# Optimization experiments

Hardware: AMD Instinct MI355X
Metric: run time of the kernel (lower is better)

The kernel has to match this reference:

```python
import jax, jax.numpy as jnp
import numpy as np

N, E, G = 100000, 1600000, 64
IN_DIM, EMB, HID, HEADS, OUT = 128, 128, 32, 4, 64
CAT = HID * HEADS  # 128
EPS = 1e-5
SLOPE = 0.2


def gat_conv(x, src, dst, W, a_src, a_dst, bias):
    # x: [N, F_in]; W: [HEADS*HID, F_in]; a_*: [1, HEADS, HID]; bias: [HEADS*HID]
    h = (x @ W.T).reshape(N, HEADS, HID)
    s_src = (h * a_src).sum(-1)  # [N, HEADS]
    s_dst = (h * a_dst).sum(-1)
    e = jax.nn.leaky_relu(s_src[src] + s_dst[dst], SLOPE)  # [Etot, HEADS]
    m = jax.ops.segment_max(e, dst, num_segments=N)
    p = jnp.exp(e - m[dst])
    denom = jax.ops.segment_sum(p, dst, num_segments=N)
    alpha = p / denom[dst]  # softmax over incoming edges per dst node
    out = jax.ops.segment_sum(h[src] * alpha[:, :, None], dst, num_segments=N)
    return out.reshape(N, CAT) + bias


def graph_norm(x, batch, w, b, mean_scale):
    cnt = jax.ops.segment_sum(jnp.ones((N,), x.dtype), batch, num_segments=G)[:, None]
    mean = jax.ops.segment_sum(x, batch, num_segments=G) / cnt  # [G, C]
    sub = x - mean_scale * mean[batch]
    var = jax.ops.segment_sum(sub * sub, batch, num_segments=G) / cnt
    inv = 1.0 / jnp.sqrt(var + EPS)
    return w * sub * inv[batch] + b


def setup_inputs() -> dict:
    key = jax.random.key(0)
    ks = jax.random.split(key, 20)
    g = lambda k, shape, s: jax.random.normal(k, shape, dtype=jnp.float32) * s
    inp = {
        'x': g(ks[0], (N, IN_DIM), 1.0),
        'edge_index': jax.random.randint(ks[1], (2, E), 0, N, dtype=jnp.int64 if jax.config.read('jax_enable_x64') else jnp.int32),
        'batch': jnp.sort(jax.random.randint(ks[2], (N,), 0, G)),
        'enc_w': g(ks[3], (EMB, IN_DIM), 0.08),
        'enc_b': jnp.zeros((EMB,), jnp.float32),
        'w1': g(ks[4], (HEADS * HID, EMB), 0.08),
        'att_src1': g(ks[5], (1, HEADS, HID), 0.15),
        'att_dst1': g(ks[6], (1, HEADS, HID), 0.15),
        'b1': jnp.zeros((CAT,), jnp.float32),
        'n1_w': jnp.ones((CAT,), jnp.float32),
        'n1_b': jnp.zeros((CAT,), jnp.float32),
        'n1_ms': jnp.ones((CAT,), jnp.float32),
        'w2': g(ks[7], (HEADS * HID, CAT), 0.08),
        'att_src2': g(ks[8], (1, HEADS, HID), 0.15),
        'att_dst2': g(ks[9], (1, HEADS, HID), 0.15),
        'b2': jnp.zeros((CAT,), jnp.float32),
        'n2_w': jnp.ones((CAT,), jnp.float32),
        'n2_b': jnp.zeros((CAT,), jnp.float32),
        'n2_ms': jnp.ones((CAT,), jnp.float32),
        'fc_w': g(ks[10], (OUT, CAT), 0.08),
        'fc_b': jnp.zeros((OUT,), jnp.float32),
    }
    return inp


def reference(x, edge_index, batch, enc_w, enc_b, w1, att_src1, att_dst1, b1,
              n1_w, n1_b, n1_ms, w2, att_src2, att_dst2, b2, n2_w, n2_b, n2_ms,
              fc_w, fc_b):
    # PyG GATConv adds self-loops by default
    loops = jnp.arange(N, dtype=edge_index.dtype)
    src = jnp.concatenate([edge_index[0], loops])
    dst = jnp.concatenate([edge_index[1], loops])

    h = x @ enc_w.T + enc_b
    h = jax.nn.elu(gat_conv(h, src, dst, w1, att_src1, att_dst1, b1))
    h = graph_norm(h, batch, n1_w, n1_b, n1_ms)  # dropout = identity (eval)
    h = jax.nn.elu(gat_conv(h, src, dst, w2, att_src2, att_dst2, b2))
    h = graph_norm(h, batch, n2_w, n2_b, n2_ms)
    pooled = jax.ops.segment_max(h, batch, num_segments=G)  # global_max_pool
    return pooled @ fc_w.T + fc_b  # out_dim != 1 -> no sigmoid
```

## Files before the change

### kernel.cpp

```cpp
#include <hip/hip_runtime.h>
#include <hip/hip_bf16.h>

#define SLOPE 0.2f
#define EPS_GN 1e-5f
#define APITCH 136
#define NBUCK 391

typedef __attribute__((ext_vector_type(8))) short bfrag;
typedef __attribute__((ext_vector_type(4))) float ffrag;

__device__ __forceinline__ float lrelu(float v) { return v > 0.f ? v : SLOPE * v; }
__device__ __forceinline__ unsigned int flipf(float x) {
    unsigned int u = __float_as_uint(x);
    return (u & 0x80000000u) ? ~u : (u | 0x80000000u);
}
__device__ __forceinline__ float unflipf(unsigned int u) {
    return __uint_as_float((u & 0x80000000u) ? (u & 0x7fffffffu) : ~u);
}
__device__ __forceinline__ short f2bs(float v) {
    __hip_bfloat16 h = __float2bfloat16(v);
    return *reinterpret_cast<short*>(&h);
}
__device__ __forceinline__ float bs2f(short s) {
    __hip_bfloat16 h = *reinterpret_cast<__hip_bfloat16*>(&s);
    return __bfloat162float(h);
}
__device__ __forceinline__ float blo(unsigned int u) { return __uint_as_float(u << 16); }
__device__ __forceinline__ float bhi(unsigned int u) { return __uint_as_float(u & 0xffff0000u); }

__global__ void zero_kernel(float* __restrict__ p, int n) {
    int i = blockIdx.x * 256 + threadIdx.x;
    if (i < n) p[i] = 0.f;
}

__global__ void prep_weights(const float* __restrict__ enc_w,
                             const float* __restrict__ enc_b,
                             const float* __restrict__ w1,
                             const float* __restrict__ w2,
                             unsigned short* __restrict__ WT1b,
                             unsigned short* __restrict__ WT2b,
                             float* __restrict__ bc1, float* __restrict__ bc2) {
    int c = blockIdx.x;
    int k = threadIdx.x;
    __shared__ float w1row[128];
    w1row[k] = w1[c * 128 + k];
    __syncthreads();
    float acc = 0.f;
    for (int j = 0; j < 128; ++j)
        acc = fmaf(w1row[j], enc_w[j * 128 + k], acc);
    WT1b[c * 128 + k] = (unsigned short)f2bs(acc);
    WT2b[c * 128 + k] = (unsigned short)f2bs(w2[c * 128 + k]);
    if (k == 0) {
        float b = 0.f;
        for (int j = 0; j < 128; ++j) b += w1row[j] * enc_b[j];
        bc1[c] = b;
        bc2[c] = 0.f;
    }
}


__global__ void __launch_bounds__(256) bucket_hist(const int* __restrict__ ei,
                                                   int* __restrict__ bhist, int E, int N) {
    __shared__ int h[NBUCK];
    for (int i = threadIdx.x; i < NBUCK; i += 256) h[i] = 0;
    __syncthreads();
    int base = blockIdx.x * 4096;
#pragma unroll
    for (int s = 0; s < 16; ++s) {
        int e = base + s * 256 + threadIdx.x;
        if (e < E + N) {
            int dst = (e < E) ? ei[E + e] : (e - E);
            atomicAdd(&h[dst >> 8], 1);
        }
    }
    __syncthreads();
    for (int i = threadIdx.x; i < NBUCK; i += 256)
        if (h[i]) atomicAdd(&bhist[i], h[i]);
}

__global__ void bucket_scan(const int* __restrict__ bhist,
                            int* __restrict__ bbase, int* __restrict__ bcur) {
    __shared__ int sh[512];
    int t = threadIdx.x;
    int v = (t < NBUCK) ? bhist[t] : 0;
    sh[t] = v;
    __syncthreads();
    for (int off = 1; off < 512; off <<= 1) {
        int add = (t >= off) ? sh[t - off] : 0;
        __syncthreads();
        sh[t] += add;
        __syncthreads();
    }
    if (t < NBUCK) {
        bbase[t] = sh[t] - v;
        bcur[t] = sh[t] - v;
    }
}

__global__ void __launch_bounds__(256) bucket_scatter(const int* __restrict__ ei,
                                                      int* __restrict__ bcur,
                                                      unsigned int* __restrict__ staging,
                                                      int E, int N) {
    __shared__ int h[NBUCK];
    __shared__ int lb[NBUCK];
    for (int i = threadIdx.x; i < NBUCK; i += 256) h[i] = 0;
    __syncthreads();
    int base = blockIdx.x * 4096;
    int srcv[16], dstv[16];
#pragma unroll
    for (int s = 0; s < 16; ++s) {
        int e = base + s * 256 + threadIdx.x;
        srcv[s] = -1;
        if (e < E + N) {
            srcv[s] = (e < E) ? ei[e] : (e - E);
            dstv[s] = (e < E) ? ei[E + e] : (e - E);
            atomicAdd(&h[dstv[s] >> 8], 1);
        }
    }
    __syncthreads();
    for (int i = threadIdx.x; i < NBUCK; i += 256) {
        int c = h[i];
        lb[i] = c ? atomicAdd(&bcur[i], c) : 0;
        h[i] = 0;
    }
    __syncthreads();
#pragma unroll
    for (int s = 0; s < 16; ++s) {
        if (srcv[s] >= 0) {
            int b = dstv[s] >> 8;
            int slot = atomicAdd(&h[b], 1);
            staging[lb[b] + slot] = ((unsigned int)srcv[s] << 8) | (unsigned int)(dstv[s] & 255);
        }
    }
}

__global__ void __launch_bounds__(256) bucket_finalize(
    const unsigned int* __restrict__ staging,
    const int* __restrict__ bbase, const int* __restrict__ bcur,
    int* __restrict__ rowp, int* __restrict__ esrc, int N, int Etot) {
    int b = blockIdx.x, t = threadIdx.x;
    __shared__ int h[256], sc[256];
    h[t] = 0;
    __syncthreads();
    int s0 = bbase[b], s1 = bcur[b];
    for (int j = s0 + t; j < s1; j += 256)
        atomicAdd(&h[staging[j] & 255], 1);
    __syncthreads();
    int d = h[t];
    sc[t] = d;
    __syncthreads();
    for (int off = 1; off < 256; off <<= 1) {
        int add = (t >= off) ? sc[t - off] : 0;
        __syncthreads();
        sc[t] += add;
        __syncthreads();
    }
    int excl = s0 + sc[t] - d;
    int node = b * 256 + t;
    if (node < N) rowp[node] = excl;
    if (b == 0 && t == 0) rowp[N] = Etot;
    __syncthreads();
    h[t] = excl;
    __syncthreads();
    for (int j = s0 + t; j < s1; j += 256) {
        unsigned int p = staging[j];
        int pos = atomicAdd(&h[p & 255], 1);
        esrc[pos] = (int)(p >> 8);
    }
}

__global__ void __launch_bounds__(256) gemm_mfma(
    const void* __restrict__ Ain, const unsigned short* __restrict__ WTb,
    const float* __restrict__ bias, const float* __restrict__ att_src,
    const float* __restrict__ att_dst, const int* __restrict__ batch,
    const float* __restrict__ Ac, const float* __restrict__ Bc,
    unsigned int* __restrict__ H, float* __restrict__ ssrc, float* __restrict__ sdst, int N) {
    __shared__ short Bsh[128 * APITCH];
    __shared__ short Ash[64 * APITCH];
    __shared__ float asrc_s[128], adst_s[128], bias_s[128];
    int tid = threadIdx.x;
    int base = blockIdx.x * 64;

    for (int idx = tid; idx < 2048; idx += 256) {
        int c = idx >> 4, k8 = (idx & 15) * 8;
        uint4 wv = ((const uint4*)WTb)[idx];
        *(uint4*)&Bsh[c * APITCH + k8] = wv;
    }
    if (Ac == nullptr) {
        const float* A = (const float*)Ain;
        for (int idx = tid; idx < 2048; idx += 256) {
            int nl = idx >> 5, k4 = (idx & 31) * 4;
            int node = base + nl;
            float4 v = make_float4(0.f, 0.f, 0.f, 0.f);
            if (node < N) v = ((const float4*)A)[node * 32 + (idx & 31)];
            *(short4*)&Ash[nl * APITCH + k4] =
                make_short4(f2bs(v.x), f2bs(v.y), f2bs(v.z), f2bs(v.w));
        }
    } else {
        const uint4* A4 = (const uint4*)Ain;
        for (int idx = tid; idx < 1024; idx += 256) {
            int nl = idx >> 4, u4 = idx & 15, k8 = u4 * 8;
            int node = base + nl;
            short o[8] = {0, 0, 0, 0, 0, 0, 0, 0};
            if (node < N) {
                uint4 hb = A4[node * 16 + u4];
                int g = batch[node];
                float4 a0 = *(const float4*)&Ac[g * 128 + k8];
                float4 a1 = *(const float4*)&Ac[g * 128 + k8 + 4];
                float4 b0 = *(const float4*)&Bc[g * 128 + k8];
                float4 b1 = *(const float4*)&Bc[g * 128 + k8 + 4];
                o[0] = f2bs(fmaf(blo(hb.x), a0.x, b0.x));
                o[1] = f2bs(fmaf(bhi(hb.x), a0.y, b0.y));
                o[2] = f2bs(fmaf(blo(hb.y), a0.z, b0.z));
                o[3] = f2bs(fmaf(bhi(hb.y), a0.w, b0.w));
                o[4] = f2bs(fmaf(blo(hb.z), a1.x, b1.x));
                o[5] = f2bs(fmaf(bhi(hb.z), a1.y, b1.y));
                o[6] = f2bs(fmaf(blo(hb.w), a1.z, b1.z));
                o[7] = f2bs(fmaf(bhi(hb.w), a1.w, b1.w));
            }
            *(bfrag*)&Ash[nl * APITCH + k8] = *(bfrag*)o;
        }
    }
    if (tid < 128) {
        asrc_s[tid] = att_src[tid];
        adst_s[tid] = att_dst[tid];
        bias_s[tid] = bias[tid];
    }
    __syncthreads();

    int w = tid >> 6, lane = tid & 63, col = lane & 15, quad = lane >> 4;
    int rowBase = w * 16;

    bfrag afr[4];
#pragma unroll
    for (int s = 0; s < 4; ++s)
        afr[s] = *(const bfrag*)&Ash[(rowBase + col) * APITCH + s * 32 + quad * 8];

    ffrag acc[8];
#pragma unroll
    for (int t = 0; t < 8; ++t) acc[t] = (ffrag){0.f, 0.f, 0.f, 0.f};

#pragma unroll
    for (int t = 0; t < 8; ++t) {
#pragma unroll
        for (int s = 0; s < 4; ++s) {
            bfrag bfr = *(const bfrag*)&Bsh[(t * 16 + col) * APITCH + s * 32 + quad * 8];
            acc[t] = __builtin_amdgcn_mfma_f32_16x16x32_bf16(afr[s], bfr, acc[t], 0, 0, 0);
        }
    }

#pragma unroll
    for (int t = 0; t < 8; ++t) {
        int ch = t * 16 + col;
        float bv = bias_s[ch];
#pragma unroll
        for (int r = 0; r < 4; ++r)
            Ash[(rowBase + quad * 4 + r) * APITCH + ch] = f2bs(acc[t][r] + bv);
    }
    __syncthreads();

    float2 av = make_float2(asrc_s[lane * 2], asrc_s[lane * 2 + 1]);
    float2 dv = make_float2(adst_s[lane * 2], adst_s[lane * 2 + 1]);
    for (int r = 0; r < 16; ++r) {
        int node = base + rowBase + r;
        unsigned int hb = *(const unsigned int*)&Ash[(rowBase + r) * APITCH + lane * 2];
        float hx = blo(hb);
        float hy = bhi(hb);
        float vs = hx * av.x + hy * av.y;
        float vd = hx * dv.x + hy * dv.y;
#pragma unroll
        for (int off = 8; off; off >>= 1) {
            vs += __shfl_xor(vs, off, 16);
            vd += __shfl_xor(vd, off, 16);
        }
        if (node < N) {
            H[node * 64 + lane] = hb;
            if ((lane & 15) == 0) {
                int h = lane >> 4;
                ssrc[node * 4 + h] = vs;
                sdst[node * 4 + h] = vd;
            }
        }
    }
}

__global__ void __launch_bounds__(256) agg_kernel(
    const int* __restrict__ row, const int* __restrict__ esrc,
    const float* __restrict__ ssrc, const float* __restrict__ sdst,
    const uint4* __restrict__ H4, const float* __restrict__ bias,
    uint4* __restrict__ out, int N) {
    int n = (blockIdx.x * 256 + threadIdx.x) >> 6;
    int lane = threadIdx.x & 63;
    if (n >= N) return;
    int slot = lane >> 4, li = lane & 15, head = li >> 2;
    int beg = row[n], end = row[n + 1];
    int last = end - 1;
    float sdh = sdst[n * 4 + head];
    int e0 = beg + slot;

    float num[8] = {0.f, 0.f, 0.f, 0.f, 0.f, 0.f, 0.f, 0.f};
    float den = 0.f;

    int sA = esrc[min(e0, last)];
    float svA = ssrc[sA * 4 + head];
    uint4 hbA = H4[sA * 16 + li];
    int sB = esrc[min(e0 + 4, last)];

    for (int e = e0; e < end; e += 4) {
        float svB = ssrc[sB * 4 + head];
        uint4 hbB = H4[sB * 16 + li];
        int sC = esrc[min(e + 8, last)];
        float al = __expf(lrelu(svA + sdh));
        den += al;
        num[0] = fmaf(al, blo(hbA.x), num[0]);
        num[1] = fmaf(al, bhi(hbA.x), num[1]);
        num[2] = fmaf(al, blo(hbA.y), num[2]);
        num[3] = fmaf(al, bhi(hbA.y), num[3]);
        num[4] = fmaf(al, blo(hbA.z), num[4]);
        num[5] = fmaf(al, bhi(hbA.z), num[5]);
        num[6] = fmaf(al, blo(hbA.w), num[6]);
        num[7] = fmaf(al, bhi(hbA.w), num[7]);
        svA = svB;
        hbA = hbB;
        sB = sC;
    }
    den += __shfl_xor(den, 16);
    den += __shfl_xor(den, 32);
#pragma unroll
    for (int j = 0; j < 8; ++j) {
        num[j] += __shfl_xor(num[j], 16);
        num[j] += __shfl_xor(num[j], 32);
    }
    if (slot == 0) {
        float rh = 1.f / den;
        int c0 = li * 8;
        unsigned int o[4];
#pragma unroll
        for (int p = 0; p < 4; ++p) {
            float v0 = fmaf(num[2 * p], rh, bias[c0 + 2 * p]);
            float v1 = fmaf(num[2 * p + 1], rh, bias[c0 + 2 * p + 1]);
            v0 = v0 > 0.f ? v0 : __expf(v0) - 1.f;
            v1 = v1 > 0.f ? v1 : __expf(v1) - 1.f;
            o[p] = ((unsigned int)(unsigned short)f2bs(v0)) |
                   (((unsigned int)(unsigned short)f2bs(v1)) << 16);
        }
        out[n * 16 + li] = make_uint4(o[0], o[1], o[2], o[3]);
    }
}

__global__ void norm_stats(const short* __restrict__ X, const int* __restrict__ batch,
                           float* __restrict__ gsum, float* __restrict__ gsq,
                           int* __restrict__ gcnt, int N, int countFlag) {
    int c = threadIdx.x;
    int base = blockIdx.x * 64;
    if (base >= N) return;
    int end = min(base + 64, N);
    int cur = batch[base];
    float s = 0.f, q = 0.f;
    int cnt = 0;
    for (int n = base; n < end; ++n) {
        int g = batch[n];
        if (g != cur) {
            atomicAdd(&gsum[cur * 128 + c], s);
            atomicAdd(&gsq[cur * 128 + c], q);
            if (c == 0 && countFlag) atomicAdd(&gcnt[cur], cnt);
            s = 0.f; q = 0.f; cnt = 0; cur = g;
        }
        float v = bs2f(X[n * 128 + c]);
        s += v;
        q += v * v;
        ++cnt;
    }
    atomicAdd(&gsum[cur * 128 + c], s);
    atomicAdd(&gsq[cur * 128 + c], q);
    if (c == 0 && countFlag) atomicAdd(&gcnt[cur], cnt);
}

__global__ void norm_coef(const float* __restrict__ gsum, const float* __restrict__ gsq,
                          const int* __restrict__ gcnt,
                          const float* __restrict__ w, const float* __restrict__ b,
                          const float* __restrict__ ms,
                          float* __restrict__ Ac, float* __restrict__ Bc) {
    int g = blockIdx.x, c = threadIdx.x;
    int i = g * 128 + c;
    float cntv = (float)gcnt[g];
    if (cntv < 0.5f) { Ac[i] = 0.f; Bc[i] = 0.f; return; }
    float mean = gsum[i] / cntv;
    float msv = ms[c];
    float var = gsq[i] / cntv - msv * (2.f - msv) * mean * mean;
    var = fmaxf(var, 0.f);
    float inv = rsqrtf(var + EPS_GN);
    float wv = w[c];
    Ac[i] = wv * inv;
    Bc[i] = b[c] - msv * mean * wv * inv;
}

__global__ void norm_pool(const short* __restrict__ X, const int* __restrict__ batch,
                          const float* __restrict__ Ac, const float* __restrict__ Bc,
                          unsigned int* __restrict__ pool, int N) {
    int c = threadIdx.x;
    int base = blockIdx.x * 64;
    if (base >= N) return;
    int end = min(base + 64, N);
    int cur = batch[base];
    float mx = -3e38f;
    for (int n = base; n < end; ++n) {
        int g = batch[n];
        if (g != cur) {
            atomicMax(&pool[cur * 128 + c], flipf(mx));
            mx = -3e38f;
            cur = g;
        }
        float v = fmaf(bs2f(X[n * 128 + c]), Ac[g * 128 + c], Bc[g * 128 + c]);
        mx = fmaxf(mx, v);
    }
    atomicMax(&pool[cur * 128 + c], flipf(mx));
}

__global__ void fc_kernel(const unsigned int* __restrict__ pool,
                          const float* __restrict__ fcw,
                          const float* __restrict__ fcb,
                          float* __restrict__ out) {
    int g = blockIdx.x, o = threadIdx.x;
    __shared__ float p[128];
    p[o] = unflipf(pool[g * 128 + o]);
    p[o + 64] = unflipf(pool[g * 128 + 64 + o]);
    __syncthreads();
    float acc = fcb[o];
    for (int k = 0; k < 128; ++k)
        acc = fmaf(p[k], fcw[o * 128 + k], acc);
    out[g * 64 + o] = acc;
}

extern "C" void kernel_launch(void* const* d_in, const int* in_sizes, int n_in,
                              void* d_out, int out_size, void* d_ws, size_t ws_size,
                              hipStream_t stream) {
    const float* x     = (const float*)d_in[0];
    const int* ei      = (const int*)d_in[1];
    const int* batch   = (const int*)d_in[2];
    const float* enc_w = (const float*)d_in[3];
    const float* enc_b = (const float*)d_in[4];
    const float* w1    = (const float*)d_in[5];
    const float* as1   = (const float*)d_in[6];
    const float* ad1   = (const float*)d_in[7];
    const float* b1    = (const float*)d_in[8];
    const float* n1w   = (const float*)d_in[9];
    const float* n1b   = (const float*)d_in[10];
    const float* n1ms  = (const float*)d_in[11];
    const float* w2    = (const float*)d_in[12];
    const float* as2   = (const float*)d_in[13];
    const float* ad2   = (const float*)d_in[14];
    const float* b2    = (const float*)d_in[15];
    const float* n2w   = (const float*)d_in[16];
    const float* n2b   = (const float*)d_in[17];
    const float* n2ms  = (const float*)d_in[18];
    const float* fcw   = (const float*)d_in[19];
    const float* fcb   = (const float*)d_in[20];
    float* out = (float*)d_out;

    int N = in_sizes[2];
    int E = in_sizes[1] / 2;
    int Etot = E + N;

    char* ws = (char*)d_ws;
    size_t off = 0;
    auto take = [&](size_t bytes) {
        char* p = ws + off;
        off = (off + bytes + 255) & ~(size_t)255;
        return p;
    };
    unsigned short* WT1b = (unsigned short*)take(128 * 128 * 2);
    unsigned short* WT2b = (unsigned short*)take(128 * 128 * 2);
    float* bc1 = (float*)take(512);
    float* bc2 = (float*)take(512);
    float* ssrc = (float*)take((size_t)N * 16);
    float* sdst = (float*)take((size_t)N * 16);
    int* rowp   = (int*)take((size_t)(N + 1) * 4);
    int* esrc   = (int*)take((size_t)Etot * 4);
    unsigned int* staging = (unsigned int*)take((size_t)Etot * 4);
    int* bbase  = (int*)take(512 * 4);
    int* bcur   = (int*)take(512 * 4);
    unsigned int* H = (unsigned int*)take((size_t)N * 256);
    unsigned int* AG = (unsigned int*)take((size_t)N * 256);
    float* Ac   = (float*)take(64 * 128 * 4);
    float* Bc   = (float*)take(64 * 128 * 4);
    size_t zbeg = off;
    int* bhist   = (int*)take(512 * 4);
    float* gsumA = (float*)take(64 * 128 * 4);
    float* gsqA  = (float*)take(64 * 128 * 4);
    float* gsumB = (float*)take(64 * 128 * 4);
    float* gsqB  = (float*)take(64 * 128 * 4);
    int* gcnt    = (int*)take(256);
    unsigned int* pool = (unsigned int*)take(64 * 128 * 4);
    size_t zend = off;
    if (off > ws_size) return;

    int zn = (int)((zend - zbeg) / 4);
    int EB = (Etot + 4095) / 4096;

    zero_kernel<<<(zn + 255) / 256, 256, 0, stream>>>((float*)(ws + zbeg), zn);
    prep_weights<<<128, 128, 0, stream>>>(enc_w, enc_b, w1, w2, WT1b, WT2b, bc1, bc2);

    bucket_hist<<<EB, 256, 0, stream>>>(ei, bhist, E, N);
    bucket_scan<<<1, 512, 0, stream>>>(bhist, bbase, bcur);
    bucket_scatter<<<EB, 256, 0, stream>>>(ei, bcur, staging, E, N);
    bucket_finalize<<<NBUCK, 256, 0, stream>>>(staging, bbase, bcur, rowp, esrc, N, Etot);

    gemm_mfma<<<(N + 63) / 64, 256, 0, stream>>>(x, WT1b, bc1, as1, ad1, batch,
                                                 nullptr, nullptr, H, ssrc, sdst, N);
    agg_kernel<<<(N + 3) / 4, 256, 0, stream>>>(rowp, esrc, ssrc, sdst,
                                                (const uint4*)H, b1, (uint4*)AG, N);
    norm_stats<<<(N + 63) / 64, 128, 0, stream>>>((const short*)AG, batch, gsumA, gsqA, gcnt, N, 1);
    norm_coef<<<64, 128, 0, stream>>>(gsumA, gsqA, gcnt, n1w, n1b, n1ms, Ac, Bc);

    gemm_mfma<<<(N + 63) / 64, 256, 0, stream>>>(AG, WT2b, bc2, as2, ad2, batch,
                                                 Ac, Bc, H, ssrc, sdst, N);
    agg_kernel<<<(N + 3) / 4, 256, 0, stream>>>(rowp, esrc, ssrc, sdst,
                                                (const uint4*)H, b2, (uint4*)AG, N);
    norm_stats<<<(N + 63) / 64, 128, 0, stream>>>((const short*)AG, batch, gsumB, gsqB, gcnt, N, 0);
    norm_coef<<<64, 128, 0, stream>>>(gsumB, gsqB, gcnt, n2w, n2b, n2ms, Ac, Bc);
    norm_pool<<<(N + 63) / 64, 128, 0, stream>>>((const short*)AG, batch, Ac, Bc, pool, N);

    fc_kernel<<<64, 64, 0, stream>>>(pool, fcw, fcb, out);
}
```

Measured before the change: 472.3 us.

## Fuse graph-norm statistics and max-pool into GAT aggregation kernel

The aggregation kernel now processes 64 nodes per block, 16 per wave, and accumulates per-graph sum and sum-of-squares in shared memory before flushing them with atomics. This removes the separate norm_stats passes over the aggregated features. Max pooling after the second norm is replaced by tracking the raw per-graph max and min. The fc kernel then applies the affine norm, picking max or min by the sign of the scale, so norm_pool is gone too. In exchange, the edge-loop software prefetch is dropped, there are fewer, longer-running waves, and the code assumes each 64-node block spans at most two graphs.

After: 533.7 us. 1.13x slower.

```diff
diff --git a/kernel.cpp b/kernel.cpp
--- a/kernel.cpp
+++ b/kernel.cpp
@@ -20,10 +20,6 @@
 __device__ __forceinline__ short f2bs(float v) {
     __hip_bfloat16 h = __float2bfloat16(v);
     return *reinterpret_cast<short*>(&h);
-}
-__device__ __forceinline__ float bs2f(short s) {
-    __hip_bfloat16 h = *reinterpret_cast<__hip_bfloat16*>(&s);
-    return __bfloat162float(h);
 }
 __device__ __forceinline__ float blo(unsigned int u) { return __uint_as_float(u << 16); }
 __device__ __forceinline__ float bhi(unsigned int u) { return __uint_as_float(u & 0xffff0000u); }
@@ -284,96 +280,162 @@
     }
 }
 
+template <int POOL>
 __global__ void __launch_bounds__(256) agg_kernel(
     const int* __restrict__ row, const int* __restrict__ esrc,
     const float* __restrict__ ssrc, const float* __restrict__ sdst,
     const uint4* __restrict__ H4, const float* __restrict__ bias,
-    uint4* __restrict__ out, int N) {
-    int n = (blockIdx.x * 256 + threadIdx.x) >> 6;
-    int lane = threadIdx.x & 63;
-    if (n >= N) return;
+    uint4* __restrict__ out, const int* __restrict__ batch,
+    float* __restrict__ gsum, float* __restrict__ gsq, int* __restrict__ gcnt,
+    int countFlag, unsigned int* __restrict__ rawmax,
+    unsigned int* __restrict__ rawmin, int N) {
+    __shared__ float Ls[4][2][128], Lq[4][2][128];
+    __shared__ float Lmx[4][2][128], Lmn[4][2][128];
+    __shared__ int cnt2[2];
+    int tid = threadIdx.x, w = tid >> 6, lane = tid & 63;
     int slot = lane >> 4, li = lane & 15, head = li >> 2;
-    int beg = row[n], end = row[n + 1];
-    int last = end - 1;
-    float sdh = sdst[n * 4 + head];
-    int e0 = beg + slot;
-
-    float num[8] = {0.f, 0.f, 0.f, 0.f, 0.f, 0.f, 0.f, 0.f};
-    float den = 0.f;
-
-    int sA = esrc[min(e0, last)];
-    float svA = ssrc[sA * 4 + head];
-    uint4 hbA = H4[sA * 16 + li];
-    int sB = esrc[min(e0 + 4, last)];
-
-    for (int e = e0; e < end; e += 4) {
-        float svB = ssrc[sB * 4 + head];
-        uint4 hbB = H4[sB * 16 + li];
-        int sC = esrc[min(e + 8, last)];
-        float al = __expf(lrelu(svA + sdh));
-        den += al;
-        num[0] = fmaf(al, blo(hbA.x), num[0]);
-        num[1] = fmaf(al, bhi(hbA.x), num[1]);
-        num[2] = fmaf(al, blo(hbA.y), num[2]);
-        num[3] = fmaf(al, bhi(hbA.y), num[3]);
-        num[4] = fmaf(al, blo(hbA.z), num[4]);
-        num[5] = fmaf(al, bhi(hbA.z), num[5]);
-        num[6] = fmaf(al, blo(hbA.w), num[6]);
-        num[7] = fmaf(al, bhi(hbA.w), num[7]);
-        svA = svB;
-        hbA = hbB;
-        sB = sC;
-    }
-    den += __shfl_xor(den, 16);
-    den += __shfl_xor(den, 32);
-#pragma unroll
-    for (int j = 0; j < 8; ++j) {
-        num[j] += __shfl_xor(num[j], 16);
-        num[j] += __shfl_xor(num[j], 32);
-    }
+    int base = blockIdx.x * 64;
+    int g0 = batch[base];
+    int g1 = batch[min(base + 63, N - 1)];
+    if (tid < 2) cnt2[tid] = 0;
+    int c0 = li * 8;
+    float bv[8];
+#pragma unroll
+    for (int p = 0; p < 8; ++p) bv[p] = bias[c0 + p];
+
     if (slot == 0) {
-        float rh = 1.f / den;
-        int c0 = li * 8;
-        unsigned int o[4];
-#pragma unroll
-        for (int p = 0; p < 4; ++p) {
-            float v0 = fmaf(num[2 * p], rh, bias[c0 + 2 * p]);
-            float v1 = fmaf(num[2 * p + 1], rh, bias[c0 + 2 * p + 1]);
-            v0 = v0 > 0.f ? v0 : __expf(v0) - 1.f;
-            v1 = v1 > 0.f ? v1 : __expf(v1) - 1.f;
-            o[p] = ((unsigned int)(unsigned short)f2bs(v0)) |
-                   (((unsigned int)(unsigned short)f2bs(v1)) << 16);
-        }
-        out[n * 16 + li] = make_uint4(o[0], o[1], o[2], o[3]);
-    }
-}
-
-__global__ void norm_stats(const short* __restrict__ X, const int* __restrict__ batch,
-                           float* __restrict__ gsum, float* __restrict__ gsq,
-                           int* __restrict__ gcnt, int N, int countFlag) {
-    int c = threadIdx.x;
-    int base = blockIdx.x * 64;
-    if (base >= N) return;
-    int end = min(base + 64, N);
-    int cur = batch[base];
-    float s = 0.f, q = 0.f;
-    int cnt = 0;
-    for (int n = base; n < end; ++n) {
-        int g = batch[n];
-        if (g != cur) {
-            atomicAdd(&gsum[cur * 128 + c], s);
-            atomicAdd(&gsq[cur * 128 + c], q);
-            if (c == 0 && countFlag) atomicAdd(&gcnt[cur], cnt);
-            s = 0.f; q = 0.f; cnt = 0; cur = g;
-        }
-        float v = bs2f(X[n * 128 + c]);
-        s += v;
-        q += v * v;
-        ++cnt;
-    }
-    atomicAdd(&gsum[cur * 128 + c], s);
-    atomicAdd(&gsq[cur * 128 + c], q);
-    if (c == 0 && countFlag) atomicAdd(&gcnt[cur], cnt);
+#pragma unroll
+        for (int p = 0; p < 8; ++p) {
+            Ls[w][0][c0 + p] = 0.f; Ls[w][1][c0 + p] = 0.f;
+            Lq[w][0][c0 + p] = 0.f; Lq[w][1][c0 + p] = 0.f;
+            if (POOL) {
+                Lmx[w][0][c0 + p] = -3e38f; Lmx[w][1][c0 + p] = -3e38f;
+                Lmn[w][0][c0 + p] =  3e38f; Lmn[w][1][c0 + p] =  3e38f;
+            }
+        }
+    }
+
+    float sAcc[8] = {}, qAcc[8] = {};
+    float mxA[8], mnA[8];
+#pragma unroll
+    for (int p = 0; p < 8; ++p) { mxA[p] = -3e38f; mnA[p] = 3e38f; }
+    int curSet = 0;
+
+    for (int j = 0; j < 16; ++j) {
+        int n = base + w * 16 + j;
+        if (n >= N) break;
+        int beg = row[n], end = row[n + 1];
+        float sdh = sdst[n * 4 + head];
+        float num[8] = {0.f, 0.f, 0.f, 0.f, 0.f, 0.f, 0.f, 0.f};
+        float den = 0.f;
+        for (int e = beg + slot; e < end; e += 4) {
+            int s = esrc[e];
+            float al = __expf(lrelu(ssrc[s * 4 + head] + sdh));
+            uint4 hb = H4[s * 16 + li];
+            den += al;
+            num[0] = fmaf(al, blo(hb.x), num[0]);
+            num[1] = fmaf(al, bhi(hb.x), num[1]);
+            num[2] = fmaf(al, blo(hb.y), num[2]);
+            num[3] = fmaf(al, bhi(hb.y), num[3]);
+            num[4] = fmaf(al, blo(hb.z), num[4]);
+            num[5] = fmaf(al, bhi(hb.z), num[5]);
+            num[6] = fmaf(al, blo(hb.w), num[6]);
+            num[7] = fmaf(al, bhi(hb.w), num[7]);
+        }
+        den += __shfl_xor(den, 16);
+        den += __shfl_xor(den, 32);
+#pragma unroll
+        for (int p = 0; p < 8; ++p) {
+            num[p] += __shfl_xor(num[p], 16);
+            num[p] += __shfl_xor(num[p], 32);
+        }
+        if (slot == 0) {
+            int bset = (batch[n] != g0) ? 1 : 0;
+            if (bset != curSet) {
+#pragma unroll
+                for (int p = 0; p < 8; ++p) {
+                    Ls[w][curSet][c0 + p] += sAcc[p];
+                    Lq[w][curSet][c0 + p] += qAcc[p];
+                    sAcc[p] = 0.f; qAcc[p] = 0.f;
+                    if (POOL) {
+                        Lmx[w][curSet][c0 + p] = fmaxf(Lmx[w][curSet][c0 + p], mxA[p]);
+                        Lmn[w][curSet][c0 + p] = fminf(Lmn[w][curSet][c0 + p], mnA[p]);
+                        mxA[p] = -3e38f; mnA[p] = 3e38f;
+                    }
+                }
+                curSet = bset;
+            }
+            float rh = 1.f / den;
+            unsigned int o4[4];
+#pragma unroll
+            for (int p = 0; p < 4; ++p) {
+                float v0 = fmaf(num[2 * p], rh, bv[2 * p]);
+                float v1 = fmaf(num[2 * p + 1], rh, bv[2 * p + 1]);
+                v0 = v0 > 0.f ? v0 : __expf(v0) - 1.f;
+                v1 = v1 > 0.f ? v1 : __expf(v1) - 1.f;
+                sAcc[2 * p] += v0; qAcc[2 * p] += v0 * v0;
+                sAcc[2 * p + 1] += v1; qAcc[2 * p + 1] += v1 * v1;
+                if (POOL) {
+                    mxA[2 * p] = fmaxf(mxA[2 * p], v0);
+                    mnA[2 * p] = fminf(mnA[2 * p], v0);
+                    mxA[2 * p + 1] = fmaxf(mxA[2 * p + 1], v1);
+                    mnA[2 * p + 1] = fminf(mnA[2 * p + 1], v1);
+                }
+                o4[p] = ((unsigned int)(unsigned short)f2bs(v0)) |
+                        (((unsigned int)(unsigned short)f2bs(v1)) << 16);
+            }
+            out[n * 16 + li] = make_uint4(o4[0], o4[1], o4[2], o4[3]);
+        }
+    }
+    if (slot == 0) {
+#pragma unroll
+        for (int p = 0; p < 8; ++p) {
+            Ls[w][curSet][c0 + p] += sAcc[p];
+            Lq[w][curSet][c0 + p] += qAcc[p];
+            if (POOL) {
+                Lmx[w][curSet][c0 + p] = fmaxf(Lmx[w][curSet][c0 + p], mxA[p]);
+                Lmn[w][curSet][c0 + p] = fminf(Lmn[w][curSet][c0 + p], mnA[p]);
+            }
+        }
+    }
+    __syncthreads();
+    if (countFlag && tid < 64) {
+        int n = base + tid;
+        if (n < N) atomicAdd(&cnt2[(batch[n] != g0) ? 1 : 0], 1);
+    }
+    if (tid < 128) {
+        float s0 = Ls[0][0][tid] + Ls[1][0][tid] + Ls[2][0][tid] + Ls[3][0][tid];
+        float q0 = Lq[0][0][tid] + Lq[1][0][tid] + Lq[2][0][tid] + Lq[3][0][tid];
+        atomicAdd(&gsum[g0 * 128 + tid], s0);
+        atomicAdd(&gsq[g0 * 128 + tid], q0);
+        if (POOL) {
+            float m0 = fmaxf(fmaxf(Lmx[0][0][tid], Lmx[1][0][tid]),
+                             fmaxf(Lmx[2][0][tid], Lmx[3][0][tid]));
+            float n0 = fminf(fminf(Lmn[0][0][tid], Lmn[1][0][tid]),
+                             fminf(Lmn[2][0][tid], Lmn[3][0][tid]));
+            if (m0 > -2e38f) atomicMax(&rawmax[g0 * 128 + tid], flipf(m0));
+            if (n0 < 2e38f) atomicMin(&rawmin[g0 * 128 + tid], flipf(n0));
+        }
+        if (g1 != g0) {
+            float s1 = Ls[0][1][tid] + Ls[1][1][tid] + Ls[2][1][tid] + Ls[3][1][tid];
+            float q1 = Lq[0][1][tid] + Lq[1][1][tid] + Lq[2][1][tid] + Lq[3][1][tid];
+            atomicAdd(&gsum[g1 * 128 + tid], s1);
+            atomicAdd(&gsq[g1 * 128 + tid], q1);
+            if (POOL) {
+                float m1 = fmaxf(fmaxf(Lmx[0][1][tid], Lmx[1][1][tid]),
+                                 fmaxf(Lmx[2][1][tid], Lmx[3][1][tid]));
+                float n1 = fminf(fminf(Lmn[0][1][tid], Lmn[1][1][tid]),
+                                 fminf(Lmn[2][1][tid], Lmn[3][1][tid]));
+                if (m1 > -2e38f) atomicMax(&rawmax[g1 * 128 + tid], flipf(m1));
+                if (n1 < 2e38f) atomicMin(&rawmin[g1 * 128 + tid], flipf(n1));
+            }
+        }
+    }
+    __syncthreads();
+    if (countFlag && tid < 2) {
+        int g = (tid == 0) ? g0 : g1;
+        if ((tid == 0 || g1 != g0) && cnt2[tid]) atomicAdd(&gcnt[g], cnt2[tid]);
+    }
 }
 
 __global__ void norm_coef(const float* __restrict__ gsum, const float* __restrict__ gsq,
@@ -395,36 +457,22 @@
     Bc[i] = b[c] - msv * mean * wv * inv;
 }
 
-__global__ void norm_pool(const short* __restrict__ X, const int* __restrict__ batch,
+__global__ void fc_kernel(const unsigned int* __restrict__ rawmax,
+                          const unsigned int* __restrict__ rawmin,
                           const float* __restrict__ Ac, const float* __restrict__ Bc,
-                          unsigned int* __restrict__ pool, int N) {
-    int c = threadIdx.x;
-    int base = blockIdx.x * 64;
-    if (base >= N) return;
-    int end = min(base + 64, N);
-    int cur = batch[base];
-    float mx = -3e38f;
-    for (int n = base; n < end; ++n) {
-        int g = batch[n];
-        if (g != cur) {
-            atomicMax(&pool[cur * 128 + c], flipf(mx));
-            mx = -3e38f;
-            cur = g;
-        }
-        float v = fmaf(bs2f(X[n * 128 + c]), Ac[g * 128 + c], Bc[g * 128 + c]);
-        mx = fmaxf(mx, v);
-    }
-    atomicMax(&pool[cur * 128 + c], flipf(mx));
-}
-
-__global__ void fc_kernel(const unsigned int* __restrict__ pool,
                           const float* __restrict__ fcw,
                           const float* __restrict__ fcb,
                           float* __restrict__ out) {
     int g = blockIdx.x, o = threadIdx.x;
     __shared__ float p[128];
-    p[o] = unflipf(pool[g * 128 + o]);
-    p[o + 64] = unflipf(pool[g * 128 + 64 + o]);
+#pragma unroll
+    for (int h = 0; h < 2; ++h) {
+        int c = o + h * 64;
+        float a = Ac[g * 128 + c], bb = Bc[g * 128 + c];
+        float M = unflipf(rawmax[g * 128 + c]);
+        float m = unflipf(rawmin[g * 128 + c]);
+        p[c] = (a >= 0.f) ? fmaf(a, M, bb) : fmaf(a, m, bb);
+    }
     __syncthreads();
     float acc = fcb[o];
     for (int k = 0; k < 128; ++k)
@@ -484,6 +532,7 @@
     unsigned int* AG = (unsigned int*)take((size_t)N * 256);
     float* Ac   = (float*)take(64 * 128 * 4);
     float* Bc   = (float*)take(64 * 128 * 4);
+    unsigned int* rawmin = (unsigned int*)take(64 * 128 * 4);
     size_t zbeg = off;
     int* bhist   = (int*)take(512 * 4);
     float* gsumA = (float*)take(64 * 128 * 4);
@@ -491,7 +540,7 @@
     float* gsumB = (float*)take(64 * 128 * 4);
     float* gsqB  = (float*)take(64 * 128 * 4);
     int* gcnt    = (int*)take(256);
-    unsigned int* pool = (unsigned int*)take(64 * 128 * 4);
+    unsigned int* rawmax = (unsigned int*)take(64 * 128 * 4);
     size_t zend = off;
     if (off > ws_size) return;
 
@@ -499,6 +548,7 @@
     int EB = (Etot + 4095) / 4096;
 
     zero_kernel<<<(zn + 255) / 256, 256, 0, stream>>>((float*)(ws + zbeg), zn);
+    hipMemsetAsync(rawmin, 0xFF, 64 * 128 * 4, stream);
     prep_weights<<<128, 128, 0, stream>>>(enc_w, enc_b, w1, w2, WT1b, WT2b, bc1, bc2);
 
     bucket_hist<<<EB, 256, 0, stream>>>(ei, bhist, E, N);
@@ -508,18 +558,17 @@
 
     gemm_mfma<<<(N + 63) / 64, 256, 0, stream>>>(x, WT1b, bc1, as1, ad1, batch,
                                                  nullptr, nullptr, H, ssrc, sdst, N);
-    agg_kernel<<<(N + 3) / 4, 256, 0, stream>>>(rowp, esrc, ssrc, sdst,
-                                                (const uint4*)H, b1, (uint4*)AG, N);
-    norm_stats<<<(N + 63) / 64, 128, 0, stream>>>((const short*)AG, batch, gsumA, gsqA, gcnt, N, 1);
+    agg_kernel<0><<<(N + 63) / 64, 256, 0, stream>>>(
+        rowp, esrc, ssrc, sdst, (const uint4*)H, b1, (uint4*)AG, batch,
+        gsumA, gsqA, gcnt, 1, nullptr, nullptr, N);
     norm_coef<<<64, 128, 0, stream>>>(gsumA, gsqA, gcnt, n1w, n1b, n1ms, Ac, Bc);
 
     gemm_mfma<<<(N + 63) / 64, 256, 0, stream>>>(AG, WT2b, bc2, as2, ad2, batch,
                                                  Ac, Bc, H, ssrc, sdst, N);
-    agg_kernel<<<(N + 3) / 4, 256, 0, stream>>>(rowp, esrc, ssrc, sdst,
-                                                (const uint4*)H, b2, (uint4*)AG, N);
-    norm_stats<<<(N + 63) / 64, 128, 0, stream>>>((const short*)AG, batch, gsumB, gsqB, gcnt, N, 0);
+    agg_kernel<1><<<(N + 63) / 64, 256, 0, stream>>>(
+        rowp, esrc, ssrc, sdst, (const uint4*)H, b2, (uint4*)AG, batch,
+        gsumB, gsqB, gcnt, 0, rawmax, rawmin, N);
     norm_coef<<<64, 128, 0, stream>>>(gsumB, gsqB, gcnt, n2w, n2b, n2ms, Ac, Bc);
-    norm_pool<<<(N + 63) / 64, 128, 0, stream>>>((const short*)AG, batch, Ac, Bc, pool, N);
-
-    fc_kernel<<<64, 64, 0, stream>>>(pool, fcw, fcb, out);
-}
+
+    fc_kernel<<<64, 64, 0, stream>>>(rawmax, rawmin, Ac, Bc, fcw, fcb, out);
+}
```
